# Optimization experiments

Hardware: AMD Instinct MI355X
Metric: run time of the kernel (lower is better)

## Reference

```python
import jax, jax.numpy as jnp
import numpy as np

INPUT_SIZE = 32
HIDDEN = 64
BATCH = 4096
SEQ = 256


def setup_inputs() -> dict:
    key = jax.random.key(0)
    ks = jax.random.split(key, 7)
    s_ih = 1.0 / np.sqrt(HIDDEN)
    # PyTorch nn.RNN init: U(-1/sqrt(H), 1/sqrt(H)) for all params
    return {
        "x": jax.random.normal(ks[0], (BATCH, SEQ, INPUT_SIZE), jnp.float32),
        "W_ih": jax.random.uniform(ks[1], (HIDDEN, INPUT_SIZE), jnp.float32, -s_ih, s_ih),
        "W_hh": jax.random.uniform(ks[2], (HIDDEN, HIDDEN), jnp.float32, -s_ih, s_ih),
        "b_ih": jax.random.uniform(ks[3], (HIDDEN,), jnp.float32, -s_ih, s_ih),
        "b_hh": jax.random.uniform(ks[4], (HIDDEN,), jnp.float32, -s_ih, s_ih),
        "W_fc": jax.random.uniform(ks[5], (1, HIDDEN), jnp.float32, -s_ih, s_ih),
        "b_fc": jax.random.uniform(ks[6], (1,), jnp.float32, -s_ih, s_ih),
    }


def reference(x, W_ih, W_hh, b_ih, b_hh, W_fc, b_fc):
    # Precompute input projection for all timesteps: [B, T, H]
    xW = jnp.einsum("bti,hi->bth", x, W_ih) + b_ih + b_hh
    xW_t = jnp.swapaxes(xW, 0, 1)  # [T, B, H] for scan over time

    def step(h, xw_t):
        h_new = jnp.tanh(xw_t + h @ W_hh.T)
        return h_new, None

    h0 = jnp.zeros((x.shape[0], W_hh.shape[0]), x.dtype)
    h_last, _ = jax.lax.scan(step, h0, xW_t)
    # Dropout is identity in eval mode; take last timestep hidden -> linear head
    return h_last @ W_fc.T + b_fc  # [B, 1]
```

## Files before the change

kernel.cpp:

```cpp
#include <hip/hip_runtime.h>

#define INPUT 32
#define HIDDEN 64
#define BATCH 4096
#define SEQ 256

typedef __attribute__((ext_vector_type(8))) short bf16x8;
typedef __attribute__((ext_vector_type(4))) float floatx4;

#define MFMA(a, b, c) __builtin_amdgcn_mfma_f32_16x16x32_bf16((a), (b), (c), 0, 0, 0)

#define LDS_BARRIER() asm volatile("s_waitcnt lgkmcnt(0)\n\ts_barrier" ::: "memory")

__device__ __forceinline__ unsigned short f2bf(float f) {
    unsigned u = __float_as_uint(f);
    u += 0x7fffu + ((u >> 16) & 1u);
    return (unsigned short)(u >> 16);
}
__device__ __forceinline__ float bf2f(unsigned short b) {
    return __uint_as_float(((unsigned)b) << 16);
}
__device__ __forceinline__ void split8(const float f[8], bf16x8& hi, bf16x8& lo) {
#pragma unroll
    for (int j = 0; j < 8; ++j) {
        unsigned short h = f2bf(f[j]);
        hi[j] = (short)h;
        lo[j] = (short)f2bf(f[j] - bf2f(h));
    }
}

__device__ __forceinline__ void packpair(float f0, float f1, unsigned& hw, unsigned& lw) {
    unsigned b0 = __float_as_uint(f0), b1 = __float_as_uint(f1);
    float h0 = __uint_as_float(b0 & 0xffff0000u);
    float h1 = __uint_as_float(b1 & 0xffff0000u);
    float l0 = f0 - h0, l1 = f1 - h1;
    hw = __builtin_amdgcn_perm(b1, b0, 0x07060302u);
    lw = __builtin_amdgcn_perm(__float_as_uint(l1), __float_as_uint(l0), 0x07060302u);
}

__device__ __forceinline__ unsigned pack_rne(float f0, float f1) {
    unsigned r0 = __float_as_uint(f0);
    r0 += 0x7fffu + ((r0 >> 16) & 1u);
    unsigned r1 = __float_as_uint(f1);
    r1 += 0x7fffu + ((r1 >> 16) & 1u);
    return __builtin_amdgcn_perm(r1, r0, 0x07060302u);
}

union FragU { bf16x8 v; unsigned u[4]; };

__global__ __launch_bounds__(256, 1) void rnn_ns2_kernel(
    const float* __restrict__ x,
    const float* __restrict__ W_ih,
    const float* __restrict__ W_hh,
    const float* __restrict__ b_ih,
    const float* __restrict__ b_hh,
    const float* __restrict__ W_fc,
    const float* __restrict__ b_fc,
    float* __restrict__ out)
{
    const int tid  = threadIdx.x;
    const int nt   = tid >> 6;
    const int lane = tid & 63;
    const int ln   = lane & 15;
    const int qd   = lane >> 4;
    const int b0   = blockIdx.x * 16;

    __shared__ __align__(16) unsigned short Gs[2048];
    __shared__ float Ps[64];

    {
        unsigned* z = (unsigned*)Gs;
        for (int i = tid; i < 512; i += 256) z[i] = 0u;
    }

    const int mrow = nt * 16 + ln;
    bf16x8 WihH, WihL, WhhH[2], WhhL[2];
    {
        float f[8];
        const float* ri = W_ih + mrow * INPUT + qd * 8;
        *(float4*)&f[0] = *(const float4*)ri;
        *(float4*)&f[4] = *(const float4*)(ri + 4);
        split8(f, WihH, WihL);
        const float* rh = W_hh + mrow * HIDDEN + qd * 8;
#pragma unroll
        for (int kt = 0; kt < 2; ++kt) {
            *(float4*)&f[0] = *(const float4*)(rh + kt * 32);
            *(float4*)&f[4] = *(const float4*)(rh + kt * 32 + 4);
            split8(f, WhhH[kt], WhhL[kt]);
        }
    }
    const int u0 = nt * 16 + qd * 4;
    floatx4 bbv, wfcv;
    {
        float4 bi = *(const float4*)(b_ih + u0);
        float4 bh = *(const float4*)(b_hh + u0);
        bbv[0] = bi.x + bh.x; bbv[1] = bi.y + bh.y;
        bbv[2] = bi.z + bh.z; bbv[3] = bi.w + bh.w;
        float4 wf = *(const float4*)(W_fc + u0);
        wfcv[0] = wf.x; wfcv[1] = wf.y; wfcv[2] = wf.z; wfcv[3] = wf.w;
    }

    const int rbase = ln * 32 + ((qd + (ln >> 1)) & 3) * 8;
    const int wbase = (u0 >> 5) * 512 + ln * 32 +
                      ((((u0 >> 3) & 3) + (ln >> 1)) & 3) * 8 + (u0 & 7);

    const float* xp = x + (size_t)(b0 + ln) * (SEQ * INPUT) + qd * 8;

    float4 xa[4], xb[4];
#pragma unroll
    for (int i = 0; i < 4; ++i) {
        xa[i] = *(const float4*)(xp + i * INPUT);
        xb[i] = *(const float4*)(xp + i * INPUT + 4);
    }

    floatx4 ihacc;
    {
        FragU xH, xL;
        packpair(xa[0].x, xa[0].y, xH.u[0], xL.u[0]);
        packpair(xa[0].z, xa[0].w, xH.u[1], xL.u[1]);
        packpair(xb[0].x, xb[0].y, xH.u[2], xL.u[2]);
        packpair(xb[0].z, xb[0].w, xH.u[3], xL.u[3]);
        ihacc = MFMA(WihH, xH.v, bbv);
        ihacc = MFMA(WihH, xL.v, ihacc);
        ihacc = MFMA(WihL, xH.v, ihacc);
    }

    __syncthreads();

    bf16x8 g0 = *(const bf16x8*)(Gs + rbase);
    bf16x8 g1 = *(const bf16x8*)(Gs + rbase + 512);

    float hv[4];

#pragma unroll 1
    for (int tb = 0; tb < SEQ; tb += 4) {
#pragma unroll
        for (int s = 0; s < 4; ++s) {
            const int t = tb + s;
            const int tn = (t + 4 < SEQ) ? t + 4 : SEQ - 1;
            xa[s] = *(const float4*)(xp + tn * INPUT);
            xb[s] = *(const float4*)(xp + tn * INPUT + 4);

            const float4 na = xa[(s + 1) & 3], nb = xb[(s + 1) & 3];
            FragU nxH, nxL;
            packpair(na.x, na.y, nxH.u[0], nxL.u[0]);
            packpair(na.z, na.w, nxH.u[1], nxL.u[1]);
            packpair(nb.x, nb.y, nxH.u[2], nxL.u[2]);
            packpair(nb.z, nb.w, nxH.u[3], nxL.u[3]);
            floatx4 ihn = MFMA(WihH, nxH.v, bbv);
            ihn = MFMA(WihH, nxL.v, ihn);
            ihn = MFMA(WihL, nxH.v, ihn);

            floatx4 a = MFMA(WhhH[0], g0, ihacc);
            a = MFMA(WhhH[1], g1, a);
            floatx4 c = {0.f, 0.f, 0.f, 0.f};
            c = MFMA(WhhL[0], g0, c);
            c = MFMA(WhhL[1], g1, c);

#pragma unroll
            for (int r = 0; r < 4; ++r) {
                float p = a[r] + c[r];
                float e = __expf(2.0f * p);
                hv[r] = 1.0f - 2.0f * __builtin_amdgcn_rcpf(e + 1.0f);
            }

            unsigned w0 = pack_rne(hv[0], hv[1]);
            unsigned w1 = pack_rne(hv[2], hv[3]);
            uint2 wv; wv.x = w0; wv.y = w1;
            *(uint2*)(Gs + (((t & 1) ^ 1) << 10) + wbase) = wv;

            LDS_BARRIER();

            const unsigned short* Hr = Gs + (((t & 1) ^ 1) << 10) + rbase;
            g0 = *(const bf16x8*)(Hr);
            g1 = *(const bf16x8*)(Hr + 512);

            ihacc = ihn;
        }
    }

    float acc = wfcv[0] * hv[0] + wfcv[1] * hv[1] + wfcv[2] * hv[2] + wfcv[3] * hv[3];
    acc += __shfl_xor(acc, 16, 64);
    acc += __shfl_xor(acc, 32, 64);
    if (qd == 0) Ps[nt * 16 + ln] = acc;
    __syncthreads();
    if (tid < 16)
        out[b0 + tid] = Ps[tid] + Ps[16 + tid] + Ps[32 + tid] + Ps[48 + tid] + b_fc[0];
}

extern "C" void kernel_launch(void* const* d_in, const int* in_sizes, int n_in,
                              void* d_out, int out_size, void* d_ws, size_t ws_size,
                              hipStream_t stream) {
    const float* x    = (const float*)d_in[0];
    const float* W_ih = (const float*)d_in[1];
    const float* W_hh = (const float*)d_in[2];
    const float* b_ih = (const float*)d_in[3];
    const float* b_hh = (const float*)d_in[4];
    const float* W_fc = (const float*)d_in[5];
    const float* b_fc = (const float*)d_in[6];
    float* out = (float*)d_out;

    rnn_ns2_kernel<<<dim3(BATCH / 16), dim3(256), 0, stream>>>(
        x, W_ih, W_hh, b_ih, b_hh, W_fc, b_fc, out);
}
```

Before: 286.8 us.

## Stage x through LDS via async global_load_lds, one wave per timestep

Each timestep, instead of every wave loading its own x slice into registers four steps ahead, one wave issues direct global-to-LDS loads into a 4-slot ring buffer. All waves then read the slot from LDS, and the h fragment loads move to the top of each step. The aim is to cut redundant global loads across the four waves and the register pressure of holding x prefetches, in exchange for extra LDS traffic and explicit vmcnt waits tied to the barrier schedule. Correctness depends on the vmcnt wait placement matching the ring-slot reuse distance.

```diff
diff --git a/kernel.cpp b/kernel.cpp
--- a/kernel.cpp
+++ b/kernel.cpp
@@ -11,6 +11,12 @@
 #define MFMA(a, b, c) __builtin_amdgcn_mfma_f32_16x16x32_bf16((a), (b), (c), 0, 0, 0)
 
 #define LDS_BARRIER() asm volatile("s_waitcnt lgkmcnt(0)\n\ts_barrier" ::: "memory")
+
+__device__ __forceinline__ void load_lds16(const float* g, void* l) {
+    __builtin_amdgcn_global_load_lds(
+        (const __attribute__((address_space(1))) void*)g,
+        (__attribute__((address_space(3))) void*)l, 16, 0, 0);
+}
 
 __device__ __forceinline__ unsigned short f2bf(float f) {
     unsigned u = __float_as_uint(f);
@@ -48,7 +54,14 @@
 
 union FragU { bf16x8 v; unsigned u[4]; };
 
-__global__ __launch_bounds__(256, 1) void rnn_ns2_kernel(
+__device__ __forceinline__ void pack8(float4 a, float4 b, FragU& H, FragU& L) {
+    packpair(a.x, a.y, H.u[0], L.u[0]);
+    packpair(a.z, a.w, H.u[1], L.u[1]);
+    packpair(b.x, b.y, H.u[2], L.u[2]);
+    packpair(b.z, b.w, H.u[3], L.u[3]);
+}
+
+__global__ __launch_bounds__(256, 1) void rnn_ns4_kernel(
     const float* __restrict__ x,
     const float* __restrict__ W_ih,
     const float* __restrict__ W_hh,
@@ -66,6 +79,7 @@
     const int b0   = blockIdx.x * 16;
 
     __shared__ __align__(16) unsigned short Gs[2048];
+    __shared__ __align__(16) float Xs[2048];
     __shared__ float Ps[64];
 
     {
@@ -106,29 +120,22 @@
 
     const float* xp = x + (size_t)(b0 + ln) * (SEQ * INPUT) + qd * 8;
 
-    float4 xa[4], xb[4];
-#pragma unroll
-    for (int i = 0; i < 4; ++i) {
-        xa[i] = *(const float4*)(xp + i * INPUT);
-        xb[i] = *(const float4*)(xp + i * INPUT + 4);
-    }
-
     floatx4 ihacc;
     {
+        float4 x0a = *(const float4*)(xp);
+        float4 x0b = *(const float4*)(xp + 4);
         FragU xH, xL;
-        packpair(xa[0].x, xa[0].y, xH.u[0], xL.u[0]);
-        packpair(xa[0].z, xa[0].w, xH.u[1], xL.u[1]);
-        packpair(xb[0].x, xb[0].y, xH.u[2], xL.u[2]);
-        packpair(xb[0].z, xb[0].w, xH.u[3], xL.u[3]);
+        pack8(x0a, x0b, xH, xL);
         ihacc = MFMA(WihH, xH.v, bbv);
         ihacc = MFMA(WihH, xL.v, ihacc);
         ihacc = MFMA(WihL, xH.v, ihacc);
     }
+    if (nt > 0) {
+        load_lds16(xp + nt * INPUT,     &Xs[nt * 512]);
+        load_lds16(xp + nt * INPUT + 4, &Xs[nt * 512 + 256]);
+    }
 
     __syncthreads();
-
-    bf16x8 g0 = *(const bf16x8*)(Gs + rbase);
-    bf16x8 g1 = *(const bf16x8*)(Gs + rbase + 512);
 
     float hv[4];
 
@@ -137,19 +144,25 @@
 #pragma unroll
         for (int s = 0; s < 4; ++s) {
             const int t = tb + s;
-            const int tn = (t + 4 < SEQ) ? t + 4 : SEQ - 1;
-            xa[s] = *(const float4*)(xp + tn * INPUT);
-            xb[s] = *(const float4*)(xp + tn * INPUT + 4);
-
-            const float4 na = xa[(s + 1) & 3], nb = xb[(s + 1) & 3];
+
+            const unsigned short* Hr = Gs + ((t & 1) << 10) + rbase;
+            bf16x8 g0 = *(const bf16x8*)(Hr);
+            bf16x8 g1 = *(const bf16x8*)(Hr + 512);
+
+            const float* Xr = Xs + (((t + 1) & 3) << 9) + (lane << 2);
+            float4 ra = *(const float4*)(Xr);
+            float4 rb = *(const float4*)(Xr + 256);
             FragU nxH, nxL;
-            packpair(na.x, na.y, nxH.u[0], nxL.u[0]);
-            packpair(na.z, na.w, nxH.u[1], nxL.u[1]);
-            packpair(nb.x, nb.y, nxH.u[2], nxL.u[2]);
-            packpair(nb.z, nb.w, nxH.u[3], nxL.u[3]);
+            pack8(ra, rb, nxH, nxL);
             floatx4 ihn = MFMA(WihH, nxH.v, bbv);
             ihn = MFMA(WihH, nxL.v, ihn);
             ihn = MFMA(WihL, nxH.v, ihn);
+
+            if (nt == s) {
+                const int tn = (t + 4 < SEQ) ? t + 4 : SEQ - 1;
+                load_lds16(xp + tn * INPUT,     &Xs[s * 512]);
+                load_lds16(xp + tn * INPUT + 4, &Xs[s * 512 + 256]);
+            }
 
             floatx4 a = MFMA(WhhH[0], g0, ihacc);
             a = MFMA(WhhH[1], g1, a);
@@ -169,15 +182,16 @@
             uint2 wv; wv.x = w0; wv.y = w1;
             *(uint2*)(Gs + (((t & 1) ^ 1) << 10) + wbase) = wv;
 
+            ihacc = ihn;
+
+            if (nt == ((s + 2) & 3))
+                asm volatile("s_waitcnt vmcnt(0)" ::: "memory");
+
             LDS_BARRIER();
-
-            const unsigned short* Hr = Gs + (((t & 1) ^ 1) << 10) + rbase;
-            g0 = *(const bf16x8*)(Hr);
-            g1 = *(const bf16x8*)(Hr + 512);
-
-            ihacc = ihn;
         }
     }
+
+    asm volatile("s_waitcnt vmcnt(0)" ::: "memory");
 
     float acc = wfcv[0] * hv[0] + wfcv[1] * hv[1] + wfcv[2] * hv[2] + wfcv[3] * hv[3];
     acc += __shfl_xor(acc, 16, 64);
@@ -200,6 +214,6 @@
     const float* b_fc = (const float*)d_in[6];
     float* out = (float*)d_out;
 
-    rnn_ns2_kernel<<<dim3(BATCH / 16), dim3(256), 0, stream>>>(
+    rnn_ns4_kernel<<<dim3(BATCH / 16), dim3(256), 0, stream>>>(
         x, W_ih, W_hh, b_ih, b_hh, W_fc, b_fc, out);
 }
```

Result: slower. 352.1 us (+22.8%).

## Split RNN into chunked input-projection phase and recurrent phase via LDS

Applied to the files above, without the earlier changes.

Restructures the kernel into two phases per 32-step chunk. First, each wave computes the input projection for a slice of timesteps across all four hidden tiles and stores the results in a shared-memory buffer. Then the recurrence loop runs without any per-step global loads or input MFMAs, reading the precomputed projection from LDS. The aim is to take global load latency and input-projection MFMAs off the serial critical path. In exchange it adds about 128KB of LDS, a block-wide sync per chunk, and a phase in which the x loads are no longer overlapped with the recurrence.

```diff
diff --git a/kernel.cpp b/kernel.cpp
--- a/kernel.cpp
+++ b/kernel.cpp
@@ -4,6 +4,7 @@
 #define HIDDEN 64
 #define BATCH 4096
 #define SEQ 256
+#define CHT 32
 
 typedef __attribute__((ext_vector_type(8))) short bf16x8;
 typedef __attribute__((ext_vector_type(4))) float floatx4;
@@ -48,7 +49,14 @@
 
 union FragU { bf16x8 v; unsigned u[4]; };
 
-__global__ __launch_bounds__(256, 1) void rnn_ns2_kernel(
+__device__ __forceinline__ void pack8(float4 a, float4 b, FragU& H, FragU& L) {
+    packpair(a.x, a.y, H.u[0], L.u[0]);
+    packpair(a.z, a.w, H.u[1], L.u[1]);
+    packpair(b.x, b.y, H.u[2], L.u[2]);
+    packpair(b.z, b.w, H.u[3], L.u[3]);
+}
+
+__global__ __launch_bounds__(256, 1) void rnn_2ph_kernel(
     const float* __restrict__ x,
     const float* __restrict__ W_ih,
     const float* __restrict__ W_hh,
@@ -65,6 +73,7 @@
     const int qd   = lane >> 4;
     const int b0   = blockIdx.x * 16;
 
+    __shared__ __align__(16) float IH[CHT][4][256];
     __shared__ __align__(16) unsigned short Gs[2048];
     __shared__ float Ps[64];
 
@@ -73,15 +82,22 @@
         for (int i = tid; i < 512; i += 256) z[i] = 0u;
     }
 
-    const int mrow = nt * 16 + ln;
-    bf16x8 WihH, WihL, WhhH[2], WhhL[2];
+    bf16x8 WihH4[4], WihL4[4], WhhH[2], WhhL[2];
+    floatx4 bbv4[4];
     {
         float f[8];
-        const float* ri = W_ih + mrow * INPUT + qd * 8;
-        *(float4*)&f[0] = *(const float4*)ri;
-        *(float4*)&f[4] = *(const float4*)(ri + 4);
-        split8(f, WihH, WihL);
-        const float* rh = W_hh + mrow * HIDDEN + qd * 8;
+#pragma unroll
+        for (int mt = 0; mt < 4; ++mt) {
+            const float* ri = W_ih + (mt * 16 + ln) * INPUT + qd * 8;
+            *(float4*)&f[0] = *(const float4*)ri;
+            *(float4*)&f[4] = *(const float4*)(ri + 4);
+            split8(f, WihH4[mt], WihL4[mt]);
+            float4 bi = *(const float4*)(b_ih + mt * 16 + qd * 4);
+            float4 bh = *(const float4*)(b_hh + mt * 16 + qd * 4);
+            bbv4[mt][0] = bi.x + bh.x; bbv4[mt][1] = bi.y + bh.y;
+            bbv4[mt][2] = bi.z + bh.z; bbv4[mt][3] = bi.w + bh.w;
+        }
+        const float* rh = W_hh + (nt * 16 + ln) * HIDDEN + qd * 8;
 #pragma unroll
         for (int kt = 0; kt < 2; ++kt) {
             *(float4*)&f[0] = *(const float4*)(rh + kt * 32);
@@ -90,12 +106,8 @@
         }
     }
     const int u0 = nt * 16 + qd * 4;
-    floatx4 bbv, wfcv;
+    floatx4 wfcv;
     {
-        float4 bi = *(const float4*)(b_ih + u0);
-        float4 bh = *(const float4*)(b_hh + u0);
-        bbv[0] = bi.x + bh.x; bbv[1] = bi.y + bh.y;
-        bbv[2] = bi.z + bh.z; bbv[3] = bi.w + bh.w;
         float4 wf = *(const float4*)(W_fc + u0);
         wfcv[0] = wf.x; wfcv[1] = wf.y; wfcv[2] = wf.z; wfcv[3] = wf.w;
     }
@@ -105,77 +117,71 @@
                       ((((u0 >> 3) & 3) + (ln >> 1)) & 3) * 8 + (u0 & 7);
 
     const float* xp = x + (size_t)(b0 + ln) * (SEQ * INPUT) + qd * 8;
-
-    float4 xa[4], xb[4];
-#pragma unroll
-    for (int i = 0; i < 4; ++i) {
-        xa[i] = *(const float4*)(xp + i * INPUT);
-        xb[i] = *(const float4*)(xp + i * INPUT + 4);
-    }
-
+    const int ihoff = (qd * 16 + ln) * 4;
+
+    bf16x8 g0, g1;
     floatx4 ihacc;
-    {
-        FragU xH, xL;
-        packpair(xa[0].x, xa[0].y, xH.u[0], xL.u[0]);
-        packpair(xa[0].z, xa[0].w, xH.u[1], xL.u[1]);
-        packpair(xb[0].x, xb[0].y, xH.u[2], xL.u[2]);
-        packpair(xb[0].z, xb[0].w, xH.u[3], xL.u[3]);
-        ihacc = MFMA(WihH, xH.v, bbv);
-        ihacc = MFMA(WihH, xL.v, ihacc);
-        ihacc = MFMA(WihL, xH.v, ihacc);
-    }
-
-    __syncthreads();
-
-    bf16x8 g0 = *(const bf16x8*)(Gs + rbase);
-    bf16x8 g1 = *(const bf16x8*)(Gs + rbase + 512);
-
     float hv[4];
 
 #pragma unroll 1
-    for (int tb = 0; tb < SEQ; tb += 4) {
-#pragma unroll
-        for (int s = 0; s < 4; ++s) {
-            const int t = tb + s;
-            const int tn = (t + 4 < SEQ) ? t + 4 : SEQ - 1;
-            xa[s] = *(const float4*)(xp + tn * INPUT);
-            xb[s] = *(const float4*)(xp + tn * INPUT + 4);
-
-            const float4 na = xa[(s + 1) & 3], nb = xb[(s + 1) & 3];
-            FragU nxH, nxL;
-            packpair(na.x, na.y, nxH.u[0], nxL.u[0]);
-            packpair(na.z, na.w, nxH.u[1], nxL.u[1]);
-            packpair(nb.x, nb.y, nxH.u[2], nxL.u[2]);
-            packpair(nb.z, nb.w, nxH.u[3], nxL.u[3]);
-            floatx4 ihn = MFMA(WihH, nxH.v, bbv);
-            ihn = MFMA(WihH, nxL.v, ihn);
-            ihn = MFMA(WihL, nxH.v, ihn);
-
-            floatx4 a = MFMA(WhhH[0], g0, ihacc);
-            a = MFMA(WhhH[1], g1, a);
-            floatx4 c = {0.f, 0.f, 0.f, 0.f};
-            c = MFMA(WhhL[0], g0, c);
-            c = MFMA(WhhL[1], g1, c);
-
-#pragma unroll
-            for (int r = 0; r < 4; ++r) {
-                float p = a[r] + c[r];
-                float e = __expf(2.0f * p);
-                hv[r] = 1.0f - 2.0f * __builtin_amdgcn_rcpf(e + 1.0f);
+    for (int cb = 0; cb < SEQ; cb += CHT) {
+        {
+            const int tbase = cb + nt * (CHT / 4);
+#pragma unroll
+            for (int i = 0; i < CHT / 4; ++i) {
+                const int t = tbase + i;
+                float4 ra = *(const float4*)(xp + t * INPUT);
+                float4 rb = *(const float4*)(xp + t * INPUT + 4);
+                FragU H, L;
+                pack8(ra, rb, H, L);
+#pragma unroll
+                for (int mt = 0; mt < 4; ++mt) {
+                    floatx4 ih = MFMA(WihH4[mt], H.v, bbv4[mt]);
+                    ih = MFMA(WihH4[mt], L.v, ih);
+                    ih = MFMA(WihL4[mt], H.v, ih);
+                    *(floatx4*)&IH[t - cb][mt][ihoff] = ih;
+                }
             }
-
-            unsigned w0 = pack_rne(hv[0], hv[1]);
-            unsigned w1 = pack_rne(hv[2], hv[3]);
-            uint2 wv; wv.x = w0; wv.y = w1;
-            *(uint2*)(Gs + (((t & 1) ^ 1) << 10) + wbase) = wv;
-
-            LDS_BARRIER();
-
-            const unsigned short* Hr = Gs + (((t & 1) ^ 1) << 10) + rbase;
-            g0 = *(const bf16x8*)(Hr);
-            g1 = *(const bf16x8*)(Hr + 512);
-
-            ihacc = ihn;
+        }
+        __syncthreads();
+
+        if (cb == 0) {
+            g0 = *(const bf16x8*)(Gs + rbase);
+            g1 = *(const bf16x8*)(Gs + rbase + 512);
+        }
+        ihacc = *(const floatx4*)&IH[0][nt][ihoff];
+
+#pragma unroll 1
+        for (int sb = 0; sb < CHT; sb += 2) {
+#pragma unroll
+            for (int p = 0; p < 2; ++p) {
+                const int s = sb + p;
+
+                floatx4 a = MFMA(WhhH[0], g0, ihacc);
+                a = MFMA(WhhH[1], g1, a);
+                floatx4 c = {0.f, 0.f, 0.f, 0.f};
+                c = MFMA(WhhL[0], g0, c);
+                c = MFMA(WhhL[1], g1, c);
+
+#pragma unroll
+                for (int r = 0; r < 4; ++r) {
+                    float pv = a[r] + c[r];
+                    float e = __expf(2.0f * pv);
+                    hv[r] = 1.0f - 2.0f * __builtin_amdgcn_rcpf(e + 1.0f);
+                }
+
+                unsigned w0 = pack_rne(hv[0], hv[1]);
+                unsigned w1 = pack_rne(hv[2], hv[3]);
+                uint2 wv; wv.x = w0; wv.y = w1;
+                *(uint2*)(Gs + ((p ^ 1) << 10) + wbase) = wv;
+
+                LDS_BARRIER();
+
+                const unsigned short* Hr = Gs + ((p ^ 1) << 10) + rbase;
+                g0 = *(const bf16x8*)(Hr);
+                g1 = *(const bf16x8*)(Hr + 512);
+                ihacc = *(const floatx4*)&IH[(s + 1) & (CHT - 1)][nt][ihoff];
+            }
         }
     }
 
@@ -200,6 +206,6 @@
     const float* b_fc = (const float*)d_in[6];
     float* out = (float*)d_out;
 
-    rnn_ns2_kernel<<<dim3(BATCH / 16), dim3(256), 0, stream>>>(
+    rnn_2ph_kernel<<<dim3(BATCH / 16), dim3(256), 0, stream>>>(
         x, W_ih, W_hh, b_ih, b_hh, W_fc, b_fc, out);
 }
```

Measured after the change: 272.1 us. -5.1%, faster.
